# Optimization experiments

Measured on AMD Instinct MI355X. Metric: run time of the kernel, lower is better.

Reference implementation:

```python
import jax, jax.numpy as jnp
import numpy as np

EPS = 1e-10       # module eps
COS_EPS = 1e-8    # torch F.cosine_similarity norm clamp
TAO = 0.0
LIP = 0.0
SQUARED = False
DETACH_HR = True
LAMB_LIP = 1
# p = 1.0 -> np.random.random() < p is always True, so the sampling mask is baked to True.


def setup_inputs() -> dict:
    key = jax.random.key(0)
    k1, k2, k3 = jax.random.split(key, 3)
    img = jax.random.normal(k1, (256, 4, 3, 112, 112), dtype=jnp.float32)
    feat = jax.random.normal(k2, (256, 4, 512), dtype=jnp.float32)
    feat_norm = jax.random.normal(k3, (256, 4, 1), dtype=jnp.float32)
    return {"img": img, "feat": feat, "feat_norm": feat_norm}


def reference(img, feat, feat_norm):
    # img: [B, K, C, H, W], feat: [B, K, D], feat_norm: [B, K, 1]
    fn0 = feat_norm[:, 0, 0]                                   # [B]
    cond = fn0 > -TAO                                          # [B] outer if per batch row
    w = jax.lax.stop_gradient(1.0 / (jnp.exp(fn0) + EPS))      # [B] adaptive weight (detached)

    # consecutive-frame image L2 distance (full-tensor sum per frame pair)
    img_diff = jnp.sqrt(jnp.sum((img[:, 1:] - img[:, :-1]) ** 2, axis=(2, 3, 4))) + EPS  # [B, K-1]
    # skip frames identical to frame 0 (torch.equal check)
    neq = jnp.any(img[:, 1:] != img[:, 0:1], axis=(2, 3, 4))   # [B, K-1]

    fa = feat[:, :-1]                                          # [B, K-1, D] (HR side of each pair)
    fb = feat[:, 1:]                                           # [B, K-1, D]
    if DETACH_HR:
        fa = jax.lax.stop_gradient(fa)
    na = jnp.maximum(jnp.linalg.norm(fa, axis=-1), COS_EPS)
    nb = jnp.maximum(jnp.linalg.norm(fb, axis=-1), COS_EPS)
    cos = jnp.sum(fa * fb, axis=-1) / (na * nb)                # [B, K-1]

    ratio = (1.0 - cos) / img_diff - LIP
    term = ratio ** 2 if SQUARED else jnp.maximum(ratio, 0.0)
    term = term * w[:, None]

    mask = cond[:, None] & neq
    penalty = jnp.sum(jnp.where(mask, term, 0.0), axis=1)      # [B]
    adaptive_weight_list = jnp.where(cond, w, 0.0)             # [B]
    return LAMB_LIP * jnp.mean(penalty), adaptive_weight_list
```

## Files before the change

kernel.cpp:

```cpp
#include <hip/hip_runtime.h>
#include <math.h>

#define EPS 1e-10f
#define COS_EPS 1e-8f

#define NB 256
#define NF 4
#define FRAME_F4 9408

__global__ __launch_bounds__(1024) void fused(const float* __restrict__ img,
                                              const float* __restrict__ feat,
                                              const float* __restrict__ feat_norm,
                                              float* __restrict__ out) {
    const int b   = blockIdx.x;
    const int tid = threadIdx.x;

    const float4* base = (const float4*)img + (size_t)b * NF * FRAME_F4;

    float s1 = 0.f, s2 = 0.f, s3 = 0.f;
    int   n1 = 0,   n2 = 0,   n3 = 0;

    for (int idx = tid; idx < FRAME_F4; idx += 1024) {
        float4 f0 = base[idx];
        float4 f1 = base[FRAME_F4 + idx];
        float4 f2 = base[2 * FRAME_F4 + idx];
        float4 f3 = base[3 * FRAME_F4 + idx];

        float dx, dy, dz, dw;
        dx = f1.x - f0.x; dy = f1.y - f0.y; dz = f1.z - f0.z; dw = f1.w - f0.w;
        s1 += dx*dx + dy*dy + dz*dz + dw*dw;
        dx = f2.x - f1.x; dy = f2.y - f1.y; dz = f2.z - f1.z; dw = f2.w - f1.w;
        s2 += dx*dx + dy*dy + dz*dz + dw*dw;
        dx = f3.x - f2.x; dy = f3.y - f2.y; dz = f3.z - f2.z; dw = f3.w - f2.w;
        s3 += dx*dx + dy*dy + dz*dz + dw*dw;

        n1 |= (f1.x != f0.x) | (f1.y != f0.y) | (f1.z != f0.z) | (f1.w != f0.w);
        n2 |= (f2.x != f0.x) | (f2.y != f0.y) | (f2.z != f0.z) | (f2.w != f0.w);
        n3 |= (f3.x != f0.x) | (f3.y != f0.y) | (f3.z != f0.z) | (f3.w != f0.w);
    }

    for (int off = 32; off > 0; off >>= 1) {
        s1 += __shfl_down(s1, off);
        s2 += __shfl_down(s2, off);
        s3 += __shfl_down(s3, off);
        n1 |= __shfl_down(n1, off);
        n2 |= __shfl_down(n2, off);
        n3 |= __shfl_down(n3, off);
    }

    __shared__ float ls[3][16];
    __shared__ int   ln[3][16];
    const int wave = tid >> 6;
    const int lane = tid & 63;
    if (lane == 0) {
        ls[0][wave] = s1; ls[1][wave] = s2; ls[2][wave] = s3;
        ln[0][wave] = n1; ln[1][wave] = n2; ln[2][wave] = n3;
    }
    __syncthreads();

    const int p = wave;
    __shared__ float sh_term[3];
    if (p < 3) {
        float sq = (lane < 16) ? ls[p][lane] : 0.0f;
        int   nq = (lane < 16) ? ln[p][lane] : 0;

        const float4* fa = (const float4*)feat + ((size_t)b * NF + p) * 128;
        const float4* fb = fa + 128;

        float dab = 0.f, daa = 0.f, dbb = 0.f;
#pragma unroll
        for (int j = 0; j < 2; ++j) {
            float4 a  = fa[lane + 64 * j];
            float4 bb = fb[lane + 64 * j];
            dab += a.x * bb.x + a.y * bb.y + a.z * bb.z + a.w * bb.w;
            daa += a.x * a.x + a.y * a.y + a.z * a.z + a.w * a.w;
            dbb += bb.x * bb.x + bb.y * bb.y + bb.z * bb.z + bb.w * bb.w;
        }
        for (int off = 32; off > 0; off >>= 1) {
            dab += __shfl_down(dab, off);
            daa += __shfl_down(daa, off);
            dbb += __shfl_down(dbb, off);
            sq  += __shfl_down(sq, off);
            nq  |= __shfl_down(nq, off);
        }

        if (lane == 0) {
            float na   = fmaxf(sqrtf(daa), COS_EPS);
            float nb   = fmaxf(sqrtf(dbb), COS_EPS);
            float cosv = dab / (na * nb);
            float img_diff = sqrtf(sq) + EPS;
            float ratio = (1.0f - cosv) / img_diff;
            float term  = fmaxf(ratio, 0.0f);
            float fn0   = feat_norm[b * NF];
            float w     = 1.0f / (expf(fn0) + EPS);
            bool  cond  = fn0 > 0.0f;
            sh_term[p]  = (cond && nq) ? term * w : 0.0f;
        }
    }
    __syncthreads();
    if (tid == 0) {
        float fn0 = feat_norm[b * NF];
        float w   = 1.0f / (expf(fn0) + EPS);
        out[1 + b] = (fn0 > 0.0f) ? w : 0.0f;
        float pen = sh_term[0] + sh_term[1] + sh_term[2];
        atomicAdd(&out[0], pen * (1.0f / 256.0f));
    }
}

extern "C" void kernel_launch(void* const* d_in, const int* in_sizes, int n_in,
                              void* d_out, int out_size, void* d_ws, size_t ws_size,
                              hipStream_t stream) {
    const float* img       = (const float*)d_in[0];
    const float* feat      = (const float*)d_in[1];
    const float* feat_norm = (const float*)d_in[2];
    float* out = (float*)d_out;

    fused<<<NB, 1024, 0, stream>>>(img, feat, feat_norm, out);
}
```

Before: 222.2 us.

## Split image reduction across chunked blocks with a second finalize kernel

Replaces the single fused kernel (one 1024-thread block per batch row) with two kernels. The first splits each batch row's frames into 8 chunks handled by 256-thread blocks and writes per-chunk partial sums and inequality bits to workspace. The second kernel combines the partials with the cosine-similarity computation. This raises the block count from 256 to 2048 so the memory-bound reduction can fill more of the GPU, at the cost of an extra launch and a workspace round trip. The old fused path is kept as a fallback when no workspace is available.

```diff
diff --git a/kernel.cpp b/kernel.cpp
--- a/kernel.cpp
+++ b/kernel.cpp
@@ -7,6 +7,134 @@
 #define NB 256
 #define NF 4
 #define FRAME_F4 9408
+#define CHUNKS 8
+#define CHUNK_F4 (FRAME_F4 / CHUNKS)
+#define K1_THREADS 256
+
+__global__ __launch_bounds__(K1_THREADS, 8) void part1(const float* __restrict__ img,
+                                                       float4* __restrict__ ws) {
+    const int bid = blockIdx.x;
+    const int b   = bid >> 3;
+    const int c   = bid & (CHUNKS - 1);
+    const int tid = threadIdx.x;
+
+    const float4* base = (const float4*)img + (size_t)b * NF * FRAME_F4;
+    const int start = c * CHUNK_F4;
+    const int end   = start + CHUNK_F4;
+
+    float s1 = 0.f, s2 = 0.f, s3 = 0.f;
+    int   n1 = 0,   n2 = 0,   n3 = 0;
+
+#pragma unroll 2
+    for (int idx = start + tid; idx < end; idx += K1_THREADS) {
+        float4 f0 = base[idx];
+        float4 f1 = base[FRAME_F4 + idx];
+        float4 f2 = base[2 * FRAME_F4 + idx];
+        float4 f3 = base[3 * FRAME_F4 + idx];
+
+        float dx, dy, dz, dw;
+        dx = f1.x - f0.x; dy = f1.y - f0.y; dz = f1.z - f0.z; dw = f1.w - f0.w;
+        s1 += dx*dx + dy*dy + dz*dz + dw*dw;
+        dx = f2.x - f1.x; dy = f2.y - f1.y; dz = f2.z - f1.z; dw = f2.w - f1.w;
+        s2 += dx*dx + dy*dy + dz*dz + dw*dw;
+        dx = f3.x - f2.x; dy = f3.y - f2.y; dz = f3.z - f2.z; dw = f3.w - f2.w;
+        s3 += dx*dx + dy*dy + dz*dz + dw*dw;
+
+        n1 |= (f1.x != f0.x) | (f1.y != f0.y) | (f1.z != f0.z) | (f1.w != f0.w);
+        n2 |= (f2.x != f0.x) | (f2.y != f0.y) | (f2.z != f0.z) | (f2.w != f0.w);
+        n3 |= (f3.x != f0.x) | (f3.y != f0.y) | (f3.z != f0.z) | (f3.w != f0.w);
+    }
+
+    for (int off = 32; off > 0; off >>= 1) {
+        s1 += __shfl_down(s1, off);
+        s2 += __shfl_down(s2, off);
+        s3 += __shfl_down(s3, off);
+        n1 |= __shfl_down(n1, off);
+        n2 |= __shfl_down(n2, off);
+        n3 |= __shfl_down(n3, off);
+    }
+
+    __shared__ float ls[3][4];
+    __shared__ int   ln[3][4];
+    const int wave = tid >> 6;
+    const int lane = tid & 63;
+    if (lane == 0) {
+        ls[0][wave] = s1; ls[1][wave] = s2; ls[2][wave] = s3;
+        ln[0][wave] = n1; ln[1][wave] = n2; ln[2][wave] = n3;
+    }
+    __syncthreads();
+
+    if (tid == 0) {
+        float S1 = ls[0][0] + ls[0][1] + ls[0][2] + ls[0][3];
+        float S2 = ls[1][0] + ls[1][1] + ls[1][2] + ls[1][3];
+        float S3 = ls[2][0] + ls[2][1] + ls[2][2] + ls[2][3];
+        int   N1 = ln[0][0] | ln[0][1] | ln[0][2] | ln[0][3];
+        int   N2 = ln[1][0] | ln[1][1] | ln[1][2] | ln[1][3];
+        int   N3 = ln[2][0] | ln[2][1] | ln[2][2] | ln[2][3];
+        int bits = (N1 ? 1 : 0) | (N2 ? 2 : 0) | (N3 ? 4 : 0);
+        ws[bid] = make_float4(S1, S2, S3, __int_as_float(bits));
+    }
+}
+
+__global__ __launch_bounds__(192) void part2(const float* __restrict__ feat,
+                                             const float* __restrict__ feat_norm,
+                                             const float4* __restrict__ ws,
+                                             float* __restrict__ out) {
+    const int b    = blockIdx.x;
+    const int tid  = threadIdx.x;
+    const int p    = tid >> 6;
+    const int lane = tid & 63;
+
+    float sq = 0.f;
+    int   nq = 0;
+    if (lane < CHUNKS) {
+        float4 v = ws[b * CHUNKS + lane];
+        sq = (p == 0) ? v.x : (p == 1) ? v.y : v.z;
+        nq = (__float_as_int(v.w) >> p) & 1;
+    }
+
+    const float4* fa = (const float4*)feat + ((size_t)b * NF + p) * 128;
+    const float4* fb = fa + 128;
+
+    float dab = 0.f, daa = 0.f, dbb = 0.f;
+#pragma unroll
+    for (int j = 0; j < 2; ++j) {
+        float4 a  = fa[lane + 64 * j];
+        float4 bb = fb[lane + 64 * j];
+        dab += a.x * bb.x + a.y * bb.y + a.z * bb.z + a.w * bb.w;
+        daa += a.x * a.x + a.y * a.y + a.z * a.z + a.w * a.w;
+        dbb += bb.x * bb.x + bb.y * bb.y + bb.z * bb.z + bb.w * bb.w;
+    }
+    for (int off = 32; off > 0; off >>= 1) {
+        dab += __shfl_down(dab, off);
+        daa += __shfl_down(daa, off);
+        dbb += __shfl_down(dbb, off);
+        sq  += __shfl_down(sq, off);
+        nq  |= __shfl_down(nq, off);
+    }
+
+    __shared__ float sh_term[3];
+    if (lane == 0) {
+        float na   = fmaxf(sqrtf(daa), COS_EPS);
+        float nb   = fmaxf(sqrtf(dbb), COS_EPS);
+        float cosv = dab / (na * nb);
+        float img_diff = sqrtf(sq) + EPS;
+        float ratio = (1.0f - cosv) / img_diff;
+        float term  = fmaxf(ratio, 0.0f);
+        float fn0   = feat_norm[b * NF];
+        float w     = 1.0f / (expf(fn0) + EPS);
+        bool  cond  = fn0 > 0.0f;
+        sh_term[p]  = (cond && nq) ? term * w : 0.0f;
+    }
+    __syncthreads();
+    if (tid == 0) {
+        float fn0 = feat_norm[b * NF];
+        float w   = 1.0f / (expf(fn0) + EPS);
+        out[1 + b] = (fn0 > 0.0f) ? w : 0.0f;
+        float pen = sh_term[0] + sh_term[1] + sh_term[2];
+        atomicAdd(&out[0], pen * (1.0f / 256.0f));
+    }
+}
 
 __global__ __launch_bounds__(1024) void fused(const float* __restrict__ img,
                                               const float* __restrict__ feat,
@@ -115,5 +243,11 @@
     const float* feat_norm = (const float*)d_in[2];
     float* out = (float*)d_out;
 
-    fused<<<NB, 1024, 0, stream>>>(img, feat, feat_norm, out);
-}
+    const size_t ws_needed = sizeof(float4) * NB * CHUNKS;
+    if (ws_size >= ws_needed && d_ws != nullptr) {
+        part1<<<NB * CHUNKS, K1_THREADS, 0, stream>>>(img, (float4*)d_ws);
+        part2<<<NB, 192, 0, stream>>>(feat, feat_norm, (const float4*)d_ws, out);
+    } else {
+        fused<<<NB, 1024, 0, stream>>>(img, feat, feat_norm, out);
+    }
+}
```

Result: no change. 225.2 us (+1.3%).
